# Optimization experiments

Measured on AMD Instinct MI355X. Metric: run time of the kernel, lower is better.

The kernel has to match this reference:

```python
import jax, jax.numpy as jnp
import numpy as np

M = 262144          # rows of A == prod(out_shape) == 512*512
N = 262144          # cols of A == prod(x.shape)
NNZ = 8388608       # 32 nonzeros per row on average
OUT_SHAPE = (512, 512)


def setup_inputs() -> dict:
    key = jax.random.key(0)
    k1, k2, k3, k4 = jax.random.split(key, 4)
    A_rows = jax.random.randint(k1, (NNZ,), 0, M, dtype=jnp.int32)
    A_cols = jax.random.randint(k2, (NNZ,), 0, N, dtype=jnp.int32)
    A_vals = jax.random.normal(k3, (NNZ,), dtype=jnp.float32)
    x = jax.random.normal(k4, OUT_SHAPE, dtype=jnp.float32)
    return {"x": x, "A_vals": A_vals, "A_rows": A_rows, "A_cols": A_cols}


def reference(x, A_vals, A_rows, A_cols):
    # x.reshape(A.shape[1], 1); torch.sparse.mm(A, x); reshape(out_shape)
    xf = x.reshape(-1)                                   # [N]
    contrib = A_vals * jnp.take(xf, A_cols)              # [NNZ] gather + multiply
    y = jax.ops.segment_sum(contrib, A_rows, num_segments=M)  # scatter-add over rows
    return y.reshape(OUT_SHAPE).astype(jnp.float32)
```

## Files before the change

### kernel.cpp

```cpp
#include <hip/hip_runtime.h>


#define BINS         32
#define ROW_SHIFT    13
#define ROWS_PER_BIN 8192
#define ENT          2048
#define BKT_CAP      112
#define KST          114
#define VST          113
#define CUR_STRIDE   32
#define OVF_SLOT     (BINS * CUR_STRIDE)
#define OVF_CAP      65536

typedef int   __attribute__((ext_vector_type(4))) i32x4;
typedef float __attribute__((ext_vector_type(4))) f32x4;


__global__ __launch_bounds__(256) void zero_out_kernel(float* __restrict__ y, int n) {
    int i = blockIdx.x * blockDim.x + threadIdx.x;
    if (i < n) y[i] = 0.0f;
}

__global__ __launch_bounds__(256) void spmv_coo_scatter(
    const float* __restrict__ vals, const int* __restrict__ rows,
    const int* __restrict__ cols, const float* __restrict__ x,
    float* __restrict__ y, int nnz)
{
    int i = (blockIdx.x * blockDim.x + threadIdx.x) * 4;
    if (i + 3 < nnz) {
        float4 v = *reinterpret_cast<const float4*>(vals + i);
        int4   r = *reinterpret_cast<const int4*>(rows + i);
        int4   c = *reinterpret_cast<const int4*>(cols + i);
        atomicAdd(&y[r.x], v.x * x[c.x]);
        atomicAdd(&y[r.y], v.y * x[c.y]);
        atomicAdd(&y[r.z], v.z * x[c.z]);
        atomicAdd(&y[r.w], v.w * x[c.w]);
    } else {
        for (; i < nnz; ++i) atomicAdd(&y[rows[i]], vals[i] * x[cols[i]]);
    }
}


__global__ __launch_bounds__(256) void init_cursors(unsigned* __restrict__ gcur, int n) {
    int i = blockIdx.x * 256 + threadIdx.x;
    if (i < n) gcur[i] = 0u;
}

__global__ __launch_bounds__(256) void scatter_bucket_kernel(
    const int*   __restrict__ rows, const int* __restrict__ cols,
    const float* __restrict__ vals, const float* __restrict__ x, int nnz,
    unsigned* __restrict__ gcur, unsigned cap,
    unsigned short* __restrict__ okeys, float* __restrict__ ocontrib,
    uint2* __restrict__ ovf)
{
    __shared__ unsigned short skey[BINS * KST];
    __shared__ float          sval[BINS * VST];
    __shared__ unsigned cur[BINS];
    __shared__ unsigned scnt[BINS];
    __shared__ unsigned resv[BINS];

    const int t = threadIdx.x;
    if (t < BINS) cur[t] = 0u;
    __syncthreads();

    const int seg = blockIdx.x * ENT;

    int   rr[8];
    float ff[8];

    #pragma unroll
    for (int ch = 0; ch < 2; ++ch) {
        int base = seg + ch * 1024 + t * 4;
        if (base + 3 < nnz) {
            i32x4 r4 = __builtin_nontemporal_load(reinterpret_cast<const i32x4*>(rows + base));
            i32x4 c4 = __builtin_nontemporal_load(reinterpret_cast<const i32x4*>(cols + base));
            f32x4 v4 = __builtin_nontemporal_load(reinterpret_cast<const f32x4*>(vals + base));
            rr[ch*4+0] = r4.x; ff[ch*4+0] = v4.x * x[c4.x];
            rr[ch*4+1] = r4.y; ff[ch*4+1] = v4.y * x[c4.y];
            rr[ch*4+2] = r4.z; ff[ch*4+2] = v4.z * x[c4.z];
            rr[ch*4+3] = r4.w; ff[ch*4+3] = v4.w * x[c4.w];
        } else {
            #pragma unroll
            for (int j = 0; j < 4; ++j) {
                int idx = base + j;
                if (idx < nnz) { rr[ch*4+j] = rows[idx]; ff[ch*4+j] = vals[idx] * x[cols[idx]]; }
                else           { rr[ch*4+j] = -1; ff[ch*4+j] = 0.0f; }
            }
        }
    }

    #pragma unroll
    for (int j = 0; j < 8; ++j) {
        if (rr[j] >= 0) {
            int b = rr[j] >> ROW_SHIFT;
            unsigned p = atomicAdd(&cur[b], 1u);
            if (p < BKT_CAP) {
                skey[b * KST + p] = (unsigned short)(rr[j] & (ROWS_PER_BIN - 1));
                sval[b * VST + p] = ff[j];
            } else {
                unsigned q = atomicAdd(&gcur[OVF_SLOT], 1u);
                if (q < OVF_CAP) ovf[q] = make_uint2((unsigned)rr[j], __float_as_uint(ff[j]));
            }
        }
    }
    __syncthreads();

    if (t < BINS) {
        unsigned c = cur[t]; if (c > BKT_CAP) c = BKT_CAP;
        scnt[t] = c;
        resv[t] = atomicAdd(&gcur[t * CUR_STRIDE], c);
    }
    __syncthreads();

    const int wave = t >> 6, lane = t & 63;
    #pragma unroll
    for (int k = 0; k < BINS / 4; ++k) {
        int b = wave * (BINS / 4) + k;
        unsigned cnt  = scnt[b];
        unsigned base = resv[b];
        const size_t binoff = (size_t)b * cap;
        for (unsigned i = lane; i < cnt; i += 64) {
            unsigned off = base + i;
            if (off < cap) {
                okeys[binoff + off]    = skey[b * KST + i];
                ocontrib[binoff + off] = sval[b * VST + i];
            }
        }
    }
}

__global__ __launch_bounds__(512) void accum2_kernel(
    const unsigned short* __restrict__ okeys, const float* __restrict__ ocontrib,
    const unsigned* __restrict__ gcur, unsigned cap,
    const uint2* __restrict__ ovf,
    float* __restrict__ partials, int slices)
{
    __shared__ float acc[ROWS_PER_BIN];
    const int t   = threadIdx.x;
    const int bin = blockIdx.x / slices;
    const int sl  = blockIdx.x - bin * slices;

    float4 z = make_float4(0.f, 0.f, 0.f, 0.f);
    #pragma unroll
    for (int i = 0; i < ROWS_PER_BIN / (512 * 4); ++i)
        *reinterpret_cast<float4*>(&acc[(i * 512 + t) * 4]) = z;
    __syncthreads();

    unsigned count = gcur[bin * CUR_STRIDE];
    if (count > cap) count = cap;
    unsigned chunk = ((count + (unsigned)slices - 1u) / (unsigned)slices + 3u) & ~3u;
    unsigned lo = (unsigned)sl * chunk;
    unsigned hi = lo + chunk; if (hi > count) hi = count;

    const unsigned short* k = okeys    + (size_t)bin * cap;
    const float*          c = ocontrib + (size_t)bin * cap;

    unsigned i = lo + (unsigned)t * 4u;
    for (; i + 3u < hi; i += 2048u) {
        ushort4 k4 = *reinterpret_cast<const ushort4*>(k + i);
        float4  c4 = *reinterpret_cast<const float4*>(c + i);
        atomicAdd(&acc[k4.x], c4.x);
        atomicAdd(&acc[k4.y], c4.y);
        atomicAdd(&acc[k4.z], c4.z);
        atomicAdd(&acc[k4.w], c4.w);
    }
    for (; i < hi; ++i) atomicAdd(&acc[k[i]], c[i]);

    if (sl == 0) {
        unsigned ovn = gcur[OVF_SLOT];
        if (ovn > OVF_CAP) ovn = OVF_CAP;
        for (unsigned j = (unsigned)t; j < ovn; j += 512u) {
            uint2 e = ovf[j];
            if ((int)(e.x >> ROW_SHIFT) == bin)
                atomicAdd(&acc[e.x & (ROWS_PER_BIN - 1)], __uint_as_float(e.y));
        }
    }
    __syncthreads();

    float* p = partials + (size_t)blockIdx.x * ROWS_PER_BIN;
    #pragma unroll
    for (int i2 = 0; i2 < ROWS_PER_BIN / (512 * 4); ++i2) {
        int l = (i2 * 512 + t) * 4;
        *reinterpret_cast<float4*>(p + l) = *reinterpret_cast<const float4*>(&acc[l]);
    }
}

__global__ __launch_bounds__(256) void reduce2_kernel(
    const float* __restrict__ partials, float* __restrict__ y, int out_size, int slices)
{
    int r0 = (blockIdx.x * 256 + threadIdx.x) * 4;
    if (r0 >= out_size) return;
    if (r0 + 3 < out_size) {
        int bin = r0 >> ROW_SHIFT, local = r0 & (ROWS_PER_BIN - 1);
        const float* p = partials + ((size_t)bin * slices) * ROWS_PER_BIN + local;
        float4 s = make_float4(0.f, 0.f, 0.f, 0.f);
        for (int j = 0; j < slices; ++j) {
            float4 v = *reinterpret_cast<const float4*>(p + (size_t)j * ROWS_PER_BIN);
            s.x += v.x; s.y += v.y; s.z += v.z; s.w += v.w;
        }
        *reinterpret_cast<float4*>(y + r0) = s;
    } else {
        for (int r = r0; r < out_size; ++r) {
            int bin = r >> ROW_SHIFT, local = r & (ROWS_PER_BIN - 1);
            const float* p = partials + ((size_t)bin * slices) * ROWS_PER_BIN + local;
            float s = 0.f;
            for (int j = 0; j < slices; ++j) s += p[(size_t)j * ROWS_PER_BIN];
            y[r] = s;
        }
    }
}

extern "C" void kernel_launch(void* const* d_in, const int* in_sizes, int n_in,
                              void* d_out, int out_size, void* d_ws, size_t ws_size,
                              hipStream_t stream) {
    const float* x    = (const float*)d_in[0];
    const float* vals = (const float*)d_in[1];
    const int*   rows = (const int*)d_in[2];
    const int*   cols = (const int*)d_in[3];
    float* y = (float*)d_out;

    const int nnz  = in_sizes[1];
    const int bins = (out_size + ROWS_PER_BIN - 1) / ROWS_PER_BIN;

    unsigned cap = (unsigned)(nnz / (bins > 0 ? bins : 1)) + 16384u;
    cap = (cap + 3u) & ~3u;

    auto align256 = [](size_t v) { return (v + 255) & ~(size_t)255; };

    int slices = 32;
    size_t off_contrib = 0, off_keys = 0, off_partials = 0, off_gcur = 0, off_ovf = 0, need = 0;
    for (int attempt = 0; attempt < 2; ++attempt) {
        off_contrib  = 0;
        off_keys     = align256(off_contrib + (size_t)BINS * cap * 4);
        off_partials = align256(off_keys + (size_t)BINS * cap * 2);
        off_gcur     = align256(off_partials + (size_t)BINS * slices * ROWS_PER_BIN * 4);
        off_ovf      = align256(off_gcur + (size_t)(OVF_SLOT + CUR_STRIDE) * 4);
        need         = align256(off_ovf + (size_t)OVF_CAP * 8);
        if (need <= ws_size) break;
        slices = 16;
    }

    const bool ok = (bins == BINS) && (need <= ws_size) && (nnz > 0) && (out_size % 4 == 0);

    if (!ok) {
        zero_out_kernel<<<(out_size + 255) / 256, 256, 0, stream>>>(y, out_size);
        spmv_coo_scatter<<<(nnz + 1023) / 1024, 256, 0, stream>>>(vals, rows, cols, x, y, nnz);
        return;
    }

    char* w = (char*)d_ws;
    float*          ocontrib = (float*)(w + off_contrib);
    unsigned short* okeys    = (unsigned short*)(w + off_keys);
    float*          partials = (float*)(w + off_partials);
    unsigned*       gcur     = (unsigned*)(w + off_gcur);
    uint2*          ovf      = (uint2*)(w + off_ovf);

    const int ncur = OVF_SLOT + 1;
    init_cursors<<<(ncur + 255) / 256, 256, 0, stream>>>(gcur, ncur);
    scatter_bucket_kernel<<<(nnz + ENT - 1) / ENT, 256, 0, stream>>>(
        rows, cols, vals, x, nnz, gcur, cap, okeys, ocontrib, ovf);
    accum2_kernel<<<BINS * slices, 512, 0, stream>>>(
        okeys, ocontrib, gcur, cap, ovf, partials, slices);
    reduce2_kernel<<<(out_size / 4 + 255) / 256, 256, 0, stream>>>(
        partials, y, out_size, slices);
}
```

Baseline: 249.9 us.

## Replace partials+reduce pass with global atomic merge and enlarge scatter tiles

Removes the partials buffer and the separate reduce kernel. Each accumulation block now atomically adds its shared-memory histogram straight into y, which the init kernel zeroes together with the cursors. The scatter kernel handles 4096 entries per block with larger per-bin shared buckets, and slices are fixed at 16. This cuts partials write/read traffic and one launch, at the cost of 16-way global float atomics per output element and nondeterministic summation order.

```diff
diff --git a/kernel.cpp b/kernel.cpp
--- a/kernel.cpp
+++ b/kernel.cpp
@@ -4,13 +4,14 @@
 #define BINS         32
 #define ROW_SHIFT    13
 #define ROWS_PER_BIN 8192
-#define ENT          2048
-#define BKT_CAP      112
-#define KST          114
-#define VST          113
+#define ENT          4096
+#define BKT_CAP      200
+#define KST          202
+#define VST          201
 #define CUR_STRIDE   32
 #define OVF_SLOT     (BINS * CUR_STRIDE)
 #define OVF_CAP      65536
+#define SLICES       16
 
 typedef int   __attribute__((ext_vector_type(4))) i32x4;
 typedef float __attribute__((ext_vector_type(4))) f32x4;
@@ -41,9 +42,12 @@
 }
 
 
-__global__ __launch_bounds__(256) void init_cursors(unsigned* __restrict__ gcur, int n) {
+__global__ __launch_bounds__(256) void init_kernel(
+    float* __restrict__ y, int n, unsigned* __restrict__ gcur, int ncur)
+{
     int i = blockIdx.x * 256 + threadIdx.x;
-    if (i < n) gcur[i] = 0u;
+    if (i < n) y[i] = 0.0f;
+    if (i < ncur) gcur[i] = 0u;
 }
 
 __global__ __launch_bounds__(256) void scatter_bucket_kernel(
@@ -65,11 +69,11 @@
 
     const int seg = blockIdx.x * ENT;
 
-    int   rr[8];
-    float ff[8];
-
-    #pragma unroll
-    for (int ch = 0; ch < 2; ++ch) {
+    int   rr[16];
+    float ff[16];
+
+    #pragma unroll
+    for (int ch = 0; ch < 4; ++ch) {
         int base = seg + ch * 1024 + t * 4;
         if (base + 3 < nnz) {
             i32x4 r4 = __builtin_nontemporal_load(reinterpret_cast<const i32x4*>(rows + base));
@@ -90,7 +94,7 @@
     }
 
     #pragma unroll
-    for (int j = 0; j < 8; ++j) {
+    for (int j = 0; j < 16; ++j) {
         if (rr[j] >= 0) {
             int b = rr[j] >> ROW_SHIFT;
             unsigned p = atomicAdd(&cur[b], 1u);
@@ -129,11 +133,11 @@
     }
 }
 
-__global__ __launch_bounds__(512) void accum2_kernel(
+__global__ __launch_bounds__(512) void accum_atomic_kernel(
     const unsigned short* __restrict__ okeys, const float* __restrict__ ocontrib,
     const unsigned* __restrict__ gcur, unsigned cap,
     const uint2* __restrict__ ovf,
-    float* __restrict__ partials, int slices)
+    float* __restrict__ y, int slices)
 {
     __shared__ float acc[ROWS_PER_BIN];
     const int t   = threadIdx.x;
@@ -177,36 +181,15 @@
     }
     __syncthreads();
 
-    float* p = partials + (size_t)blockIdx.x * ROWS_PER_BIN;
+    float* yb = y + (size_t)bin * ROWS_PER_BIN;
     #pragma unroll
     for (int i2 = 0; i2 < ROWS_PER_BIN / (512 * 4); ++i2) {
         int l = (i2 * 512 + t) * 4;
-        *reinterpret_cast<float4*>(p + l) = *reinterpret_cast<const float4*>(&acc[l]);
-    }
-}
-
-__global__ __launch_bounds__(256) void reduce2_kernel(
-    const float* __restrict__ partials, float* __restrict__ y, int out_size, int slices)
-{
-    int r0 = (blockIdx.x * 256 + threadIdx.x) * 4;
-    if (r0 >= out_size) return;
-    if (r0 + 3 < out_size) {
-        int bin = r0 >> ROW_SHIFT, local = r0 & (ROWS_PER_BIN - 1);
-        const float* p = partials + ((size_t)bin * slices) * ROWS_PER_BIN + local;
-        float4 s = make_float4(0.f, 0.f, 0.f, 0.f);
-        for (int j = 0; j < slices; ++j) {
-            float4 v = *reinterpret_cast<const float4*>(p + (size_t)j * ROWS_PER_BIN);
-            s.x += v.x; s.y += v.y; s.z += v.z; s.w += v.w;
-        }
-        *reinterpret_cast<float4*>(y + r0) = s;
-    } else {
-        for (int r = r0; r < out_size; ++r) {
-            int bin = r >> ROW_SHIFT, local = r & (ROWS_PER_BIN - 1);
-            const float* p = partials + ((size_t)bin * slices) * ROWS_PER_BIN + local;
-            float s = 0.f;
-            for (int j = 0; j < slices; ++j) s += p[(size_t)j * ROWS_PER_BIN];
-            y[r] = s;
-        }
+        float4 v = *reinterpret_cast<const float4*>(&acc[l]);
+        atomicAdd(&yb[l + 0], v.x);
+        atomicAdd(&yb[l + 1], v.y);
+        atomicAdd(&yb[l + 2], v.z);
+        atomicAdd(&yb[l + 3], v.w);
     }
 }
 
@@ -227,20 +210,14 @@
 
     auto align256 = [](size_t v) { return (v + 255) & ~(size_t)255; };
 
-    int slices = 32;
-    size_t off_contrib = 0, off_keys = 0, off_partials = 0, off_gcur = 0, off_ovf = 0, need = 0;
-    for (int attempt = 0; attempt < 2; ++attempt) {
-        off_contrib  = 0;
-        off_keys     = align256(off_contrib + (size_t)BINS * cap * 4);
-        off_partials = align256(off_keys + (size_t)BINS * cap * 2);
-        off_gcur     = align256(off_partials + (size_t)BINS * slices * ROWS_PER_BIN * 4);
-        off_ovf      = align256(off_gcur + (size_t)(OVF_SLOT + CUR_STRIDE) * 4);
-        need         = align256(off_ovf + (size_t)OVF_CAP * 8);
-        if (need <= ws_size) break;
-        slices = 16;
-    }
-
-    const bool ok = (bins == BINS) && (need <= ws_size) && (nnz > 0) && (out_size % 4 == 0);
+    size_t off_contrib  = 0;
+    size_t off_keys     = align256(off_contrib + (size_t)BINS * cap * 4);
+    size_t off_gcur     = align256(off_keys + (size_t)BINS * cap * 2);
+    size_t off_ovf      = align256(off_gcur + (size_t)(OVF_SLOT + CUR_STRIDE) * 4);
+    size_t need         = align256(off_ovf + (size_t)OVF_CAP * 8);
+
+    const bool ok = (bins == BINS) && (need <= ws_size) && (nnz > 0) &&
+                    (out_size == BINS * ROWS_PER_BIN);
 
     if (!ok) {
         zero_out_kernel<<<(out_size + 255) / 256, 256, 0, stream>>>(y, out_size);
@@ -251,16 +228,14 @@
     char* w = (char*)d_ws;
     float*          ocontrib = (float*)(w + off_contrib);
     unsigned short* okeys    = (unsigned short*)(w + off_keys);
-    float*          partials = (float*)(w + off_partials);
     unsigned*       gcur     = (unsigned*)(w + off_gcur);
     uint2*          ovf      = (uint2*)(w + off_ovf);
 
     const int ncur = OVF_SLOT + 1;
-    init_cursors<<<(ncur + 255) / 256, 256, 0, stream>>>(gcur, ncur);
+    int initn = out_size > ncur ? out_size : ncur;
+    init_kernel<<<(initn + 255) / 256, 256, 0, stream>>>(y, out_size, gcur, ncur);
     scatter_bucket_kernel<<<(nnz + ENT - 1) / ENT, 256, 0, stream>>>(
         rows, cols, vals, x, nnz, gcur, cap, okeys, ocontrib, ovf);
-    accum2_kernel<<<BINS * slices, 512, 0, stream>>>(
-        okeys, ocontrib, gcur, cap, ovf, partials, slices);
-    reduce2_kernel<<<(out_size / 4 + 255) / 256, 256, 0, stream>>>(
-        partials, y, out_size, slices);
-}
+    accum_atomic_kernel<<<BINS * SLICES, 512, 0, stream>>>(
+        okeys, ocontrib, gcur, cap, ovf, y, SLICES);
+}
```

Measured after the change: 301.2 us. 20.5% more time.
